# Kernel optimization log

Measured on AMD Instinct MI355X. Metric: run time of the kernel, lower is better.

## Reference

```python
import jax, jax.numpy as jnp
import numpy as np

D = 256       # dim
M = 50        # num_celltypes
NPATH = 65536 # path tokens (256*256)
N = M + NPATH
FF = 3        # focusing_factor
K = 5         # dwc kernel size


def find_closest_factors(num):
    for i in range(int(num ** 0.5), 0, -1):
        if num % i == 0:
            return (i, num // i)
    return (1, num)


def setup_inputs() -> dict:
    key = jax.random.key(0)
    ks = jax.random.split(key, 16)
    def w(k, shape, s=0.02):
        return jax.random.normal(k, shape, dtype=jnp.float32) * s
    z = lambda *s: jnp.zeros(s, jnp.float32)
    return {
        "x": jax.random.normal(ks[0], (1, N, D), dtype=jnp.float32),
        "W_qkv": w(ks[1], (D, 3 * D)),
        "scale_linear": w(ks[2], (1, 1, D)),
        "dwc_w": w(ks[3], (D, 1, K, K)),
        "dwc_b": w(ks[4], (D,)),
        "Wa": w(ks[5], (D, D)), "ba": z(D),
        "Wb": w(ks[6], (D, D)), "bb": z(D),
        "Wc": w(ks[7], (D, 1)), "bc": z(1),
        "W1": w(ks[8], (D, D)), "b1": z(D),
        "W2": w(ks[9], (D, D)), "b2": z(D),
        "W3a": w(ks[10], (2 * D, D)), "b3a": z(D),
        "W3b": w(ks[11], (D, D)), "b3b": z(D),
        "Wf": w(ks[12], (D, D)), "bf": z(D),
    }


def reference(x, W_qkv, scale_linear, dwc_w, dwc_b, Wa, ba, Wb, bb, Wc, bc,
              W1, b1, W2, b2, W3a, b3a, W3b, b3b, Wf, bf):
    scale = D ** -0.5
    qkv = x @ W_qkv                         # (1, N, 3D)
    q, k, v = jnp.split(qkv, 3, axis=-1)
    qc, qp = q[:, :M], q[:, M:]
    kc, kp = k[:, :M], k[:, M:]
    vc, vp = v[:, :M], v[:, M:]

    # --- softmax attention branches ---
    sa = jax.nn.softmax(jnp.einsum('bic,bjc->bij', qc * scale, kc), axis=-1)
    out_self_celltypes = sa @ vc            # (1, M, D)
    cap = jax.nn.softmax(jnp.einsum('bic,bjc->bij', qp * scale, kc), axis=-1)
    out_cross_path = cap @ vc               # (1, NPATH, D)
    cac = jax.nn.softmax(jnp.einsum('bic,bjc->bij', qc * scale, kp), axis=-1)
    out_cross_celltypes = cac @ vp          # (1, M, D)

    # --- focused linear attention on path tokens ---
    sp = jax.nn.softplus(scale_linear)
    ql = (jax.nn.relu(qp) + 1e-6) / sp
    kl = (jax.nn.relu(kp) + 1e-6) / sp
    qn = jnp.linalg.norm(ql, axis=-1, keepdims=True)
    kn = jnp.linalg.norm(kl, axis=-1, keepdims=True)
    ql = ql ** FF
    kl = kl ** FF
    ql = ql / jnp.linalg.norm(ql, axis=-1, keepdims=True) * qn
    kl = kl / jnp.linalg.norm(kl, axis=-1, keepdims=True) * kn
    zfac = 1.0 / (jnp.einsum('bic,bc->bi', ql, kl.sum(axis=1)) + 1e-6)
    kv = jnp.einsum('bjc,bjd->bcd', kl, vp)                 # (1, D, D)
    out_s = jnp.einsum('bic,bcd,bi->bid', ql, kv, zfac)     # (1, NPATH, D)

    # --- depthwise conv feature map ---
    wc, hc = find_closest_factors(NPATH)
    fm = vp.reshape(1, wc, hc, D).transpose(0, 3, 1, 2)     # b c w h
    fm = jax.lax.conv_general_dilated(
        fm, dwc_w, (1, 1), 'SAME',
        dimension_numbers=('NCHW', 'OIHW', 'NCHW'), feature_group_count=D)
    fm = fm + dwc_b[None, :, None, None]
    fm = fm.transpose(0, 2, 3, 1).reshape(1, NPATH, D)
    out_self_path = (out_s + fm) @ Wf + bf  # feamap_linear (dropout=eval)

    # --- gated attention net (shared weights, 4 calls) ---
    def gated(t):
        t = t[0]  # squeeze batch -> (n, D)
        a = jnp.tanh(t @ Wa + ba)
        g = jax.nn.sigmoid(t @ Wb + bb)
        return (a * g) @ Wc + bc  # (n, 1)

    A_cc = gated(out_cross_celltypes)
    A_cp = gated(out_cross_path)
    A_sc = gated(out_self_celltypes)
    A_sp = gated(out_self_path)

    # --- attention fusion (shared weights, 2 calls) ---
    def fuse(A1, A2, x1, x2):
        h1 = jax.nn.softmax(A1.T, axis=1) @ x1[0]   # (1, D)
        h1 = jax.nn.relu(h1 @ W1 + b1)
        h2 = jax.nn.softmax(A2.T, axis=1) @ x2[0]
        h2 = jax.nn.relu(h2 @ W2 + b2)
        f = jnp.concatenate([h1, h2], axis=1)       # (1, 2D)
        return jax.nn.relu(jax.nn.relu(f @ W3a + b3a) @ W3b + b3b)

    fusion_cross = fuse(A_cc, A_cp, out_cross_celltypes, out_cross_path)
    fusion_self = fuse(A_sc, A_sp, out_self_celltypes, out_self_path)
    return jnp.concatenate([fusion_cross, fusion_self], axis=1)  # (1, 2D)
```

## Files before the change

### kernel.cpp

```cpp
#include <hip/hip_runtime.h>
#include <hip/hip_bf16.h>
#include <math.h>


constexpr int DD = 256;
constexpr int MM = 50;
constexpr float SCL = 0.0625f;

constexpr size_t B_VPH = 0;
constexpr size_t B_QLH = (size_t)32 << 20;
constexpr size_t B_KLH = (size_t)64 << 20;
constexpr size_t B_E   = (size_t)96 << 20;
constexpr size_t B_SM  = (size_t)112 << 20;
constexpr size_t B_X   = B_SM + ((size_t)2 << 20);

constexpr size_t KLSUMR = 0;
constexpr size_t KLSUMP = 256;
constexpr size_t OCCDENP= 2304;
constexpr size_t W50P   = 2816;
constexpr size_t EDENP  = 3328;
constexpr size_t H2TP   = 3336;
constexpr size_t H2DENP = 5384;
constexpr size_t OCCRAW = 5392;
constexpr size_t ZEND   = 18192;
constexpr size_t QC     = ZEND;
constexpr size_t KC     = QC + 12800;
constexpr size_t VC     = KC + 12800;
constexpr size_t VCA    = VC + 12800;
constexpr size_t VCB    = VCA + 12800;
constexpr size_t WFA    = VCB + 12800;
constexpr size_t WFB    = WFA + 65536;
constexpr size_t BFA    = WFB + 65536;
constexpr size_t BFB    = BFA + 256;
constexpr size_t OSCB   = BFB + 256;
constexpr size_t OCCB   = OSCB + 12800;
constexpr size_t ASC    = OCCB + 12800;
constexpr size_t ACC50  = ASC + 64;
constexpr size_t SMEND  = ACC50 + 64;

constexpr size_t XT_WQKV = 0;
constexpr size_t XT_WFAT = 196608;
constexpr size_t XT_WFBT = 262144;
constexpr size_t XT_KVT  = 327680;
constexpr size_t XT_QCH  = 393216;
constexpr size_t XT_KCH  = 409600;
constexpr size_t XT_VCAT = 425984;
constexpr size_t XT_VCBT = 442368;
constexpr size_t XT_END  = 458752;
constexpr size_t WS_NEEDED = B_X + XT_END * 2;

typedef short bf16x8 __attribute__((ext_vector_type(8)));
typedef float f32x4 __attribute__((ext_vector_type(4)));

__device__ __forceinline__ float rcpf_(float x){ return __builtin_amdgcn_rcpf(x); }
__device__ __forceinline__ float fsig_(float x){ return rcpf_(1.0f + __expf(-x)); }
__device__ __forceinline__ float ftanh_(float x){ return 1.0f - 2.0f * rcpf_(__expf(2.0f * x) + 1.0f); }

__device__ __forceinline__ float bf2f(unsigned short u){
  return __uint_as_float(((unsigned int)u) << 16);
}
__device__ __forceinline__ unsigned short f2bf(float f){
  union { __hip_bfloat16 h; unsigned short u; } c;
  c.h = __float2bfloat16(f);
  return c.u;
}
__device__ __forceinline__ f32x4 mfma16(bf16x8 a, bf16x8 b, f32x4 c){
  return __builtin_amdgcn_mfma_f32_16x16x32_bf16(a, b, c, 0, 0, 0);
}

__device__ __forceinline__ float waveAllSum(float v){
  #pragma unroll
  for (int m = 1; m < 64; m <<= 1) v += __shfl_xor(v, m, 64);
  return v;
}

__device__ __forceinline__ size_t fragIdx(int n, int k, int K8){
  const int tile = n >> 4, cn = n & 15;
  const int k0 = k >> 5, kqi = (k >> 3) & 3, e = k & 7;
  return (((size_t)tile * K8 + k0) * 64 + (kqi * 16 + cn)) * 8 + e;
}

__device__ __forceinline__ int kvOff(int c, int k){
  return c * 40 + (c >> 3) * 8 + k;
}

__global__ void __launch_bounds__(256) k_prep0(const float* __restrict__ x, const float* __restrict__ Wqkv,
                                               float* qc, float* kc, float* vc,
                                               unsigned short* qch, unsigned short* kch,
                                               unsigned short* __restrict__ WT){
  const int b = blockIdx.x, t = threadIdx.x;
  if (b < 48) {
    __shared__ unsigned short Tt[64][72];
    const int bn = b % 12, bk = b / 12;
    const int n0 = bn * 64, k0g = bk * 64;
    #pragma unroll
    for (int i = 0; i < 16; i++) {
      const int k_l = (t >> 6) + i * 4;
      const int n_l = t & 63;
      Tt[n_l][k_l] = f2bf(Wqkv[(size_t)(k0g + k_l) * 768 + n0 + n_l]);
    }
    __syncthreads();
    #pragma unroll
    for (int i = 0; i < 2; i++) {
      const int fr = t * 2 + i;
      const int t_l = fr >> 7;
      const int k0_l = (fr >> 6) & 1;
      const int lane_f = fr & 63;
      const int n_l = t_l * 16 + (lane_f & 15);
      const int k_l = k0_l * 32 + (lane_f >> 4) * 8;
      const int tg = (n0 >> 4) + t_l;
      const int k0gl = (k0g >> 5) + k0_l;
      bf16x8 v = *(const bf16x8*)&Tt[n_l][k_l];
      *(bf16x8*)&WT[(((size_t)tg * 8 + k0gl) * 64 + lane_f) * 8] = v;
    }
    return;
  }
  __shared__ float xs[256];
  const int r = b - 48, j = t;
  xs[j] = x[r * DD + j];
  __syncthreads();
  float aq = 0.f, ak = 0.f, av = 0.f;
  for (int k = 0; k < DD; k++) {
    float xv = xs[k];
    aq += xv * Wqkv[k * 768 + j];
    ak += xv * Wqkv[k * 768 + 256 + j];
    av += xv * Wqkv[k * 768 + 512 + j];
  }
  qc[r * DD + j] = aq; kc[r * DD + j] = ak; vc[r * DD + j] = av;
  qch[fragIdx(r, j, 8)] = f2bf(aq);
  kch[fragIdx(r, j, 8)] = f2bf(ak);
  if (r == 0) {
    for (int c = 50; c < 64; c++) {
      qch[fragIdx(c, j, 8)] = 0;
      kch[fragIdx(c, j, 8)] = 0;
    }
  }
}

__global__ void __launch_bounds__(256) k_prep1(const float* vc, const float* Wa, const float* Wb,
                                               const float* ba, const float* bb,
                                               const float* Wf, const float* bf,
                                               float* Vca, float* Vcb,
                                               unsigned short* VcaTh, unsigned short* VcbTh,
                                               float* Wfa, float* Wfb, float* bfa, float* bfb,
                                               unsigned short* WfaTh, unsigned short* WfbTh){
  __shared__ float rs[256];
  const int b = blockIdx.x, j = threadIdx.x;
  if (b < 50) {
    const int r = b;
    rs[j] = vc[r * DD + j];
    __syncthreads();
    float a = 0.f, bv = 0.f;
    for (int k = 0; k < DD; k++) { float v = rs[k]; a += v * Wa[k * DD + j]; bv += v * Wb[k * DD + j]; }
    Vca[r * DD + j] = a; Vcb[r * DD + j] = bv;
    VcaTh[fragIdx(j, r, 2)] = f2bf(a);
    VcbTh[fragIdx(j, r, 2)] = f2bf(bv);
    if (r == 0) {
      for (int c = 50; c < 64; c++) {
        VcaTh[fragIdx(j, c, 2)] = 0;
        VcbTh[fragIdx(j, c, 2)] = 0;
      }
    }
    return;
  }
  const int bb2 = b - 50;
  const float* src; const float* Wm;
  if (bb2 < 256)      { src = Wf + bb2 * DD;         Wm = Wa; }
  else if (bb2 < 512) { src = Wf + (bb2 - 256) * DD; Wm = Wb; }
  else if (bb2 == 512){ src = bf;                    Wm = Wa; }
  else                { src = bf;                    Wm = Wb; }
  rs[j] = src[j];
  __syncthreads();
  float a = 0.f;
  for (int k = 0; k < DD; k++) a += rs[k] * Wm[k * DD + j];
  if (bb2 < 256)      { Wfa[bb2 * DD + j] = a; WfaTh[fragIdx(j, bb2, 8)] = f2bf(a); }
  else if (bb2 < 512) { Wfb[(bb2 - 256) * DD + j] = a; WfbTh[fragIdx(j, bb2 - 256, 8)] = f2bf(a); }
  else if (bb2 == 512) bfa[j] = a + ba[j];
  else bfb[j] = a + bb[j];
}

__global__ void __launch_bounds__(256) k_oscg(const float* __restrict__ qc, const float* __restrict__ kc,
                                              const float* __restrict__ vc,
                                              const float* __restrict__ Wa, const float* __restrict__ Wb,
                                              const float* __restrict__ ba, const float* __restrict__ bb,
                                              const float* __restrict__ Wc, const float* __restrict__ bc,
                                              float* __restrict__ osc, float* __restrict__ A){
  const int i = blockIdx.x, t = threadIdx.x;
  __shared__ float qs[256];
  __shared__ float P[64];
  __shared__ float red[4];
  qs[t] = qc[i * DD + t];
  __syncthreads();
  if (t < 64) {
    float s = -1e30f;
    if (t < 50) {
      float acc = 0.f;
      const float4* kr = (const float4*)&kc[t * DD];
      #pragma unroll 8
      for (int k = 0; k < 64; k++) {
        float4 kv = kr[k];
        float4 qv = *(const float4*)&qs[k * 4];
        acc += qv.x * kv.x + qv.y * kv.y + qv.z * kv.z + qv.w * kv.w;
      }
      s = acc * SCL;
    }
    float mx = s;
    #pragma unroll
    for (int m = 1; m < 64; m <<= 1) mx = fmaxf(mx, __shfl_xor(mx, m, 64));
    float e = (t < 50) ? __expf(s - mx) : 0.f;
    float den = waveAllSum(e);
    P[t] = e * rcpf_(den);
  }
  __syncthreads();
  float a = 0.f;
  for (int jj = 0; jj < 50; jj++) a += P[jj] * vc[jj * DD + t];
  osc[i * DD + t] = a;
  __syncthreads();
  qs[t] = a;
  __syncthreads();
  float u = 0.f, v = 0.f;
  for (int k = 0; k < DD; k++) { float tv = qs[k]; u += tv * Wa[k * DD + t]; v += tv * Wb[k * DD + t]; }
  float g = ftanh_(u + ba[t]) * fsig_(v + bb[t]) * Wc[t];
  g = waveAllSum(g);
  const int lane = t & 63, wv = t >> 6;
  if (lane == 0) red[wv] = g;
  __syncthreads();
  if (t == 0) A[i] = red[0] + red[1] + red[2] + red[3] + bc[0];
}

__global__ void __launch_bounds__(256) k_gated(const float* __restrict__ tin,
                                               const float* __restrict__ Wa, const float* __restrict__ Wb,
                                               const float* __restrict__ ba, const float* __restrict__ bb,
                                               const float* __restrict__ Wc, const float* __restrict__ bc,
                                               float* __restrict__ A){
  int r = blockIdx.x, j = threadIdx.x;
  __shared__ float ts[256];
  __shared__ float red[4];
  ts[j] = tin[r * DD + j];
  __syncthreads();
  float u = 0.f, v = 0.f;
  for (int k = 0; k < DD; k++) { float tv = ts[k]; u += tv * Wa[k * DD + j]; v += tv * Wb[k * DD + j]; }
  float g = ftanh_(u + ba[j]) * fsig_(v + bb[j]) * Wc[j];
  g = waveAllSum(g);
  int lane = j & 63, wv = j >> 6;
  if (lane == 0) red[wv] = g;
  __syncthreads();
  if (j == 0) A[r] = red[0] + red[1] + red[2] + red[3] + bc[0];
}

__global__ void __launch_bounds__(256) k_path1(
    const float* __restrict__ x, const unsigned short* __restrict__ WTf,
    const float* __restrict__ sln,
    const unsigned short* __restrict__ kchf, const unsigned short* __restrict__ qchf,
    const unsigned short* __restrict__ VcaTf, const unsigned short* __restrict__ VcbTf,
    const float* __restrict__ ba, const float* __restrict__ bb,
    const float* __restrict__ Wc, const float* __restrict__ bc,
    unsigned short* __restrict__ vph, unsigned short* __restrict__ qlh, unsigned short* __restrict__ klh,
    float* __restrict__ E, float* __restrict__ w50p, float* __restrict__ edenp, float* __restrict__ occdenp){
  __shared__ __align__(16) char arena[38912];
  unsigned short (*Psh)[72]   = (unsigned short (*)[72])arena;
  float (*denp)[4]            = (float (*)[4])(arena + 4608);
  unsigned short (*qpsb)[264] = (unsigned short (*)[264])(arena + 5120);
  unsigned short (*kpsb)[264] = (unsigned short (*)[264])(arena + 22016);

  const int tid = threadIdx.x;
  const int i0 = blockIdx.x * 32;
  const int part = blockIdx.x & 7;
  const int lane = tid & 63;
  const int wvv = tid >> 6;
  const int cn = lane & 15;
  const int m0 = (lane >> 4) * 4;
  const int kq = (lane >> 4) * 8;

  for (int l = tid; l < 2048; l += 256) {
    const int r = l >> 6, c4 = (l & 63) * 4;
    const float4 xv = *(const float4*)&x[(size_t)(MM + i0 + r) * DD + c4];
    ushort4 o; o.x = f2bf(xv.x); o.y = f2bf(xv.y); o.z = f2bf(xv.z); o.w = f2bf(xv.w);
    *(ushort4*)&qpsb[r][c4] = o;
  }
  __syncthreads();

  bf16x8 af0[8], af1[8];
  #pragma unroll
  for (int k0 = 0; k0 < 8; k0++) {
    af0[k0] = *(const bf16x8*)&qpsb[cn][k0 * 32 + kq];
    af1[k0] = *(const bf16x8*)&qpsb[16 + cn][k0 * 32 + kq];
  }
  __syncthreads();

  bf16x8 b0[8], b1[8];
  {
    const unsigned short* Bt = WTf + ((size_t)wvv * 8 * 64 + lane) * 8;
    #pragma unroll
    for (int k0 = 0; k0 < 8; k0++) b0[k0] = *(const bf16x8*)&Bt[(size_t)k0 * 512];
  }
  #pragma unroll 1
  for (int tt = 0; tt < 12; tt++) {
    const int t = wvv + 4 * tt;
    if (tt + 1 < 12) {
      const unsigned short* Bt = WTf + (((size_t)(t + 4) * 8) * 64 + lane) * 8;
      #pragma unroll
      for (int k0 = 0; k0 < 8; k0++) b1[k0] = *(const bf16x8*)&Bt[(size_t)k0 * 512];
    }
    f32x4 acc0 = {0.f, 0.f, 0.f, 0.f};
    f32x4 acc1 = {0.f, 0.f, 0.f, 0.f};
    #pragma unroll
    for (int k0 = 0; k0 < 8; k0++) {
      acc0 = mfma16(af0[k0], b0[k0], acc0);
      acc1 = mfma16(af1[k0], b0[k0], acc1);
    }
    if (t < 16) {
      int c = t * 16 + cn;
      #pragma unroll
      for (int i = 0; i < 4; i++) {
        qpsb[m0 + i][c] = f2bf(acc0[i]);
        qpsb[16 + m0 + i][c] = f2bf(acc1[i]);
      }
    } else if (t < 32) {
      int c = (t - 16) * 16 + cn;
      #pragma unroll
      for (int i = 0; i < 4; i++) {
        kpsb[m0 + i][c] = f2bf(acc0[i]);
        kpsb[16 + m0 + i][c] = f2bf(acc1[i]);
      }
    } else {
      int c = (t - 32) * 16 + cn;
      #pragma unroll
      for (int i = 0; i < 4; i++) {
        vph[(size_t)(i0 + m0 + i) * DD + c] = f2bf(acc0[i]);
        vph[(size_t)(i0 + 16 + m0 + i) * DD + c] = f2bf(acc1[i]);
      }
    }
    #pragma unroll
    for (int k0 = 0; k0 < 8; k0++) b0[k0] = b1[k0];
  }
  __syncthreads();

  float ep0[4], ep1[4];
  {
    f32x4 accp0 = {0.f,0.f,0.f,0.f}, accp1 = {0.f,0.f,0.f,0.f};
    f32x4 accc0 = {0.f,0.f,0.f,0.f}, accc1 = {0.f,0.f,0.f,0.f};
    const unsigned short* Bk = kchf + ((size_t)wvv * 8 * 64 + lane) * 8;
    const unsigned short* Bq = qchf + ((size_t)wvv * 8 * 64 + lane) * 8;
    #pragma unroll
    for (int k0 = 0; k0 < 8; k0++) {
      bf16x8 aq0 = *(const bf16x8*)&qpsb[cn][k0 * 32 + kq];
      bf16x8 aq1 = *(const bf16x8*)&qpsb[16 + cn][k0 * 32 + kq];
      bf16x8 ak0 = *(const bf16x8*)&kpsb[cn][k0 * 32 + kq];
      bf16x8 ak1 = *(const bf16x8*)&kpsb[16 + cn][k0 * 32 + kq];
      bf16x8 bk = *(const bf16x8*)&Bk[(size_t)k0 * 512];
      bf16x8 bq = *(const bf16x8*)&Bq[(size_t)k0 * 512];
      accp0 = mfma16(aq0, bk, accp0);
      accp1 = mfma16(aq1, bk, accp1);
      accc0 = mfma16(ak0, bq, accc0);
      accc1 = mfma16(ak1, bq, accc1);
    }
    const int col = wvv * 16 + cn;
    const bool ok = (col < 50);
    #pragma unroll
    for (int i = 0; i < 4; i++) {
      ep0[i] = ok ? __expf(accp0[i] * SCL) : 0.f;
      ep1[i] = ok ? __expf(accp1[i] * SCL) : 0.f;
    }
    float osum = 0.f;
    #pragma unroll
    for (int i = 0; i < 4; i++) {
      float ec0 = __expf(accc0[i] * SCL);
      float ec1 = __expf(accc1[i] * SCL);
      E[(size_t)(i0 + m0 + i) * 64 + col] = ok ? ec0 : 0.f;
      E[(size_t)(i0 + 16 + m0 + i) * 64 + col] = ok ? ec1 : 0.f;
      if (ok) osum += ec0 + ec1;
    }
    osum += __shfl_xor(osum, 16, 64);
    osum += __shfl_xor(osum, 32, 64);
    if (lane < 16 && ok) atomicAdd(&occdenp[part * 64 + col], osum);
    float d0[4], d1[4];
    #pragma unroll
    for (int i = 0; i < 4; i++) { d0[i] = ep0[i]; d1[i] = ep1[i]; }
    #pragma unroll
    for (int m = 1; m < 16; m <<= 1) {
      #pragma unroll
      for (int i = 0; i < 4; i++) {
        d0[i] += __shfl_xor(d0[i], m, 64);
        d1[i] += __shfl_xor(d1[i], m, 64);
      }
    }
    if (cn == 0) {
      #pragma unroll
      for (int i = 0; i < 4; i++) {
        denp[m0 + i][wvv] = d0[i];
        denp[16 + m0 + i][wvv] = d1[i];
      }
    }
  }
  __syncthreads();

  {
    const int col = wvv * 16 + cn;
    #pragma unroll
    for (int i = 0; i < 4; i++) {
      float4 dp = *(const float4*)&denp[m0 + i][0];
      Psh[m0 + i][col] = f2bf(ep0[i] * rcpf_(dp.x + dp.y + dp.z + dp.w));
      float4 dq = *(const float4*)&denp[16 + m0 + i][0];
      Psh[16 + m0 + i][col] = f2bf(ep1[i] * rcpf_(dq.x + dq.y + dq.z + dq.w));
    }
  }

  float4 sl4 = ((const float4*)sln)[lane];
  float4 rsp;
  rsp.x = rcpf_(log1pf(expf(sl4.x))); rsp.y = rcpf_(log1pf(expf(sl4.y)));
  rsp.z = rcpf_(log1pf(expf(sl4.z))); rsp.w = rcpf_(log1pf(expf(sl4.w)));
  float4 ba4 = ((const float4*)ba)[lane];
  float4 bb4 = ((const float4*)bb)[lane];
  float4 wc4 = ((const float4*)Wc)[lane];
  float bcv = bc[0];
  for (int rr = 0; rr < 8; rr++) {
    const int r = wvv * 8 + rr;
    const int row = i0 + r;
    ushort4 qu = *(const ushort4*)&qpsb[r][lane * 4];
    ushort4 ku = *(const ushort4*)&kpsb[r][lane * 4];
    float4 q4 = {bf2f(qu.x), bf2f(qu.y), bf2f(qu.z), bf2f(qu.w)};
    float4 k4 = {bf2f(ku.x), bf2f(ku.y), bf2f(ku.z), bf2f(ku.w)};
    float4 lq, lk;
    lq.x = (fmaxf(q4.x, 0.f) + 1e-6f) * rsp.x; lq.y = (fmaxf(q4.y, 0.f) + 1e-6f) * rsp.y;
    lq.z = (fmaxf(q4.z, 0.f) + 1e-6f) * rsp.z; lq.w = (fmaxf(q4.w, 0.f) + 1e-6f) * rsp.w;
    lk.x = (fmaxf(k4.x, 0.f) + 1e-6f) * rsp.x; lk.y = (fmaxf(k4.y, 0.f) + 1e-6f) * rsp.y;
    lk.z = (fmaxf(k4.z, 0.f) + 1e-6f) * rsp.z; lk.w = (fmaxf(k4.w, 0.f) + 1e-6f) * rsp.w;
    float4 q3, k3;
    q3.x = lq.x*lq.x*lq.x; q3.y = lq.y*lq.y*lq.y; q3.z = lq.z*lq.z*lq.z; q3.w = lq.w*lq.w*lq.w;
    k3.x = lk.x*lk.x*lk.x; k3.y = lk.y*lk.y*lk.y; k3.z = lk.z*lk.z*lk.z; k3.w = lk.w*lk.w*lk.w;
    float n1q = lq.x*lq.x + lq.y*lq.y + lq.z*lq.z + lq.w*lq.w;
    float n3q = q3.x*q3.x + q3.y*q3.y + q3.z*q3.z + q3.w*q3.w;
    float n1k = lk.x*lk.x + lk.y*lk.y + lk.z*lk.z + lk.w*lk.w;
    float n3k = k3.x*k3.x + k3.y*k3.y + k3.z*k3.z + k3.w*k3.w;
    n1q = waveAllSum(n1q); n3q = waveAllSum(n3q);
    n1k = waveAllSum(n1k); n3k = waveAllSum(n3k);
    float fq = sqrtf(n1q * rcpf_(n3q));
    float fk = sqrtf(n1k * rcpf_(n3k));
    ushort4 qo, ko;
    qo.x = f2bf(q3.x * fq); qo.y = f2bf(q3.y * fq); qo.z = f2bf(q3.z * fq); qo.w = f2bf(q3.w * fq);
    ko.x = f2bf(k3.x * fk); ko.y = f2bf(k3.y * fk); ko.z = f2bf(k3.z * fk); ko.w = f2bf(k3.w * fk);
    *(ushort4*)&qlh[(size_t)row * DD + lane * 4] = qo;
    *(ushort4*)&klh[(size_t)row * DD + lane * 4] = ko;
  }
  __syncthreads();

  {
    bf16x8 ap0[2], ap1[2];
    #pragma unroll
    for (int k0 = 0; k0 < 2; k0++) {
      ap0[k0] = *(const bf16x8*)&Psh[cn][k0 * 32 + kq];
      ap1[k0] = *(const bf16x8*)&Psh[16 + cn][k0 * 32 + kq];
    }
    #pragma unroll 1
    for (int tt = 0; tt < 4; tt++) {
      const int nt = wvv * 4 + tt;
      const unsigned short* Bu = VcaTf + (((size_t)nt * 2) * 64 + lane) * 8;
      const unsigned short* Bv = VcbTf + (((size_t)nt * 2) * 64 + lane) * 8;
      f32x4 au0 = {0.f,0.f,0.f,0.f}, au1 = {0.f,0.f,0.f,0.f};
      f32x4 av0 = {0.f,0.f,0.f,0.f}, av1 = {0.f,0.f,0.f,0.f};
      #pragma unroll
      for (int k0 = 0; k0 < 2; k0++) {
        bf16x8 bu = *(const bf16x8*)&Bu[(size_t)k0 * 512];
        bf16x8 bv = *(const bf16x8*)&Bv[(size_t)k0 * 512];
        au0 = mfma16(ap0[k0], bu, au0);
        au1 = mfma16(ap1[k0], bu, au1);
        av0 = mfma16(ap0[k0], bv, av0);
        av1 = mfma16(ap1[k0], bv, av1);
      }
      #pragma unroll
      for (int i = 0; i < 4; i++) {
        qpsb[m0 + i][nt * 16 + cn] = f2bf(au0[i]);
        qpsb[16 + m0 + i][nt * 16 + cn] = f2bf(au1[i]);
        kpsb[m0 + i][nt * 16 + cn] = f2bf(av0[i]);
        kpsb[16 + m0 + i][nt * 16 + cn] = f2bf(av1[i]);
      }
    }
  }
  __syncthreads();

  #pragma unroll
  for (int rr = 0; rr < 8; rr++) {
    const int r = wvv * 8 + rr;
    ushort4 uu = *(const ushort4*)&qpsb[r][lane * 4];
    ushort4 vv = *(const ushort4*)&kpsb[r][lane * 4];
    float g = ftanh_(bf2f(uu.x) + ba4.x) * fsig_(bf2f(vv.x) + bb4.x) * wc4.x
            + ftanh_(bf2f(uu.y) + ba4.y) * fsig_(bf2f(vv.y) + bb4.y) * wc4.y
            + ftanh_(bf2f(uu.z) + ba4.z) * fsig_(bf2f(vv.z) + bb4.z) * wc4.z
            + ftanh_(bf2f(uu.w) + ba4.w) * fsig_(bf2f(vv.w) + bb4.w) * wc4.w;
    g = waveAllSum(g);
    if (lane == 0) *(float*)&Psh[r][64] = __expf(g + bcv);
  }
  __syncthreads();
  if (tid < 64) {
    float s = 0.f;
    #pragma unroll
    for (int r = 0; r < 32; r++) s += *(const float*)&Psh[r][64] * bf2f(Psh[r][tid]);
    atomicAdd(&w50p[part * 64 + tid], s);
  }
  if (tid == 0) {
    float es = 0.f;
    #pragma unroll
    for (int r = 0; r < 32; r++) es += *(const float*)&Psh[r][64];
    atomicAdd(&edenp[part], es);
  }
}

__global__ void __launch_bounds__(512) k_occnum(const float* __restrict__ E, const unsigned short* __restrict__ vph,
                                                float* __restrict__ occraw){
  const int d = threadIdx.x & 255;
  const int half = threadIdx.x >> 8;
  const int j0 = blockIdx.x * 256;
  __shared__ float Es[2][32][64];
  float acc[52];
  #pragma unroll
  for (int i = 0; i < 52; i++) acc[i] = 0.f;
  for (int s = 0; s < 4; s++) {
    const int sj = j0 + (half * 4 + s) * 32;
    for (int l = d; l < 512; l += 256) {
      int jj = l >> 4, cq = l & 15;
      *(float4*)&Es[half][jj][cq * 4] = ((const float4*)(E + (size_t)(sj + jj) * 64))[cq];
    }
    __syncthreads();
    for (int jj = 0; jj < 32; jj++) {
      float vv = bf2f(vph[(size_t)(sj + jj) * DD + d]);
      #pragma unroll
      for (int q = 0; q < 13; q++) {
        float4 e4 = *(const float4*)&Es[half][jj][q * 4];
        acc[q * 4 + 0] += e4.x * vv; acc[q * 4 + 1] += e4.y * vv;
        acc[q * 4 + 2] += e4.z * vv; acc[q * 4 + 3] += e4.w * vv;
      }
    }
    __syncthreads();
  }
  for (int i = 0; i < 50; i++) atomicAdd(&occraw[i * DD + d], acc[i]);
}

__global__ void __launch_bounds__(256) k_kv(const unsigned short* __restrict__ klh,
                                            const unsigned short* __restrict__ vph,
                                            unsigned short* __restrict__ PP,
                                            float* __restrict__ klsump){
  __shared__ __align__(16) unsigned short AklT[2608];
  __shared__ __align__(16) unsigned short BvpT[10480];
  const int tid = threadIdx.x;
  const int lane = tid & 63;
  const int wvv = tid >> 6;
  const int cn = lane & 15;
  const int m0 = (lane >> 4) * 4;
  const int kq = (lane >> 4) * 8;
  const int cb = blockIdx.x;
  const int z  = blockIdx.y;
  const int jj = tid >> 3;
  const int c8 = (tid & 7) * 8;

  f32x4 acc[4][4];
  f32x4 acc1[4];
  #pragma unroll
  for (int mt = 0; mt < 4; mt++) {
    acc1[mt] = (f32x4){0.f,0.f,0.f,0.f};
    #pragma unroll
    for (int tl = 0; tl < 4; tl++) acc[mt][tl] = (f32x4){0.f,0.f,0.f,0.f};
  }
  bf16x8 ones;
  #pragma unroll
  for (int i = 0; i < 8; i++) ones[i] = (short)0x3F80;

  const int jbase = z * 512;
  #pragma unroll 1
  for (int step = 0; step < 16; step++) {
    const int j0 = jbase + step * 32;
    {
      bf16x8 av = *(const bf16x8*)&klh[(size_t)(j0 + jj) * 256 + cb * 64 + c8];
      #pragma unroll
      for (int i = 0; i < 8; i++) AklT[kvOff(c8 + i, jj)] = (unsigned short)av[i];
      #pragma unroll
      for (int rep = 0; rep < 4; rep++) {
        bf16x8 bv = *(const bf16x8*)&vph[(size_t)(j0 + jj) * 256 + rep * 64 + c8];
        #pragma unroll
        for (int i = 0; i < 8; i++) BvpT[kvOff(rep * 64 + c8 + i, jj)] = (unsigned short)bv[i];
      }
    }
    __syncthreads();
    bf16x8 afr[4], bfr[4];
    #pragma unroll
    for (int mt = 0; mt < 4; mt++)
      afr[mt] = *(const bf16x8*)&AklT[kvOff(cn + mt * 16, kq)];
    #pragma unroll
    for (int tl = 0; tl < 4; tl++)
      bfr[tl] = *(const bf16x8*)&BvpT[kvOff(wvv * 64 + tl * 16 + cn, kq)];
    #pragma unroll
    for (int mt = 0; mt < 4; mt++) {
      acc1[mt] = mfma16(afr[mt], ones, acc1[mt]);
      #pragma unroll
      for (int tl = 0; tl < 4; tl++) acc[mt][tl] = mfma16(afr[mt], bfr[tl], acc[mt][tl]);
    }
    __syncthreads();
  }
  unsigned short* P = PP + ((size_t)(cb * 128 + z)) * 16384;
  #pragma unroll
  for (int mt = 0; mt < 4; mt++)
    #pragma unroll
    for (int tl = 0; tl < 4; tl++) {
      const int n = (wvv * 4 + tl) * 16 + cn;
      #pragma unroll
      for (int i = 0; i < 4; i++)
        P[(size_t)(mt * 16 + m0 + i) * 256 + n] = f2bf(acc[mt][tl][i]);
    }
  if (wvv == 0 && cn == 0) {
    #pragma unroll
    for (int mt = 0; mt < 4; mt++)
      #pragma unroll
      for (int i = 0; i < 4; i++)
        atomicAdd(&klsump[(z & 7) * 256 + cb * 64 + mt * 16 + m0 + i], acc1[mt][i]);
  }
}

__global__ void __launch_bounds__(256) k_fin2(const unsigned short* __restrict__ PP,
                                              unsigned short* __restrict__ kvTf,
                                              const float* __restrict__ occraw,
                                              const float* __restrict__ occdenp,
                                              float* __restrict__ occ,
                                              const float* __restrict__ klsump,
                                              float* __restrict__ klsum){
  const int b = blockIdx.x, d = threadIdx.x;
  if (b < 256) {
    const int cb = b >> 6, m = b & 63;
    float s = 0.f;
    for (int z = 0; z < 128; z++)
      s += bf2f(PP[((size_t)(cb * 128 + z)) * 16384 + (size_t)m * 256 + d]);
    kvTf[fragIdx(d, b, 8)] = f2bf(s);
  } else if (b < 306) {
    const int i = b - 256;
    float den = 0.f;
    #pragma unroll
    for (int p = 0; p < 8; p++) den += occdenp[p * 64 + i];
    occ[i * DD + d] = occraw[i * DD + d] / den;
  } else {
    float s = 0.f;
    #pragma unroll
    for (int p = 0; p < 8; p++) s += klsump[p * 256 + d];
    klsum[d] = s;
  }
}

__global__ void __launch_bounds__(256) k_tail(const unsigned short* __restrict__ qlh,
                                              const unsigned short* __restrict__ kvTf,
                                              const float* __restrict__ klsum,
                                              const unsigned short* __restrict__ vph,
                                              const float* __restrict__ dwcw, const float* __restrict__ dwcb,
                                              const unsigned short* __restrict__ WfaTf,
                                              const unsigned short* __restrict__ WfbTf,
                                              const float* __restrict__ bfa, const float* __restrict__ bfb,
                                              const float* __restrict__ Wc, const float* __restrict__ bc,
                                              float* __restrict__ h2tp, float* __restrict__ h2denp){
  __shared__ unsigned short Tsh[32][264];
  __shared__ unsigned short OSb[32][264];
  __shared__ unsigned short aVb[32][264];
  __shared__ float zf[32];
  __shared__ float ev[32];
  const int tid = threadIdx.x;
  const int i0 = blockIdx.x * 32;
  const int part = blockIdx.x & 7;
  const int lane = tid & 63;
  const int wvv = tid >> 6;
  const int cn = lane & 15;
  const int m0 = (lane >> 4) * 4;
  const int kq = (lane >> 4) * 8;
  for (int l = tid; l < 2048; l += 256) {
    int r = l >> 6, c4 = (l & 63) * 4;
    *(ushort4*)&Tsh[r][c4] = *(const ushort4*)&qlh[(size_t)(i0 + r) * DD + c4];
  }
  __syncthreads();
  {
    bf16x8 afq0[8], afq1[8];
    #pragma unroll
    for (int k0 = 0; k0 < 8; k0++) {
      afq0[k0] = *(const bf16x8*)&Tsh[cn][k0 * 32 + kq];
      afq1[k0] = *(const bf16x8*)&Tsh[16 + cn][k0 * 32 + kq];
    }
    #pragma unroll 1
    for (int tt = 0; tt < 4; tt++) {
      const int nt = wvv * 4 + tt;
      const unsigned short* Bt = kvTf + (((size_t)nt * 8) * 64 + lane) * 8;
      f32x4 acc0 = {0.f,0.f,0.f,0.f};
      f32x4 acc1 = {0.f,0.f,0.f,0.f};
      #pragma unroll
      for (int k0 = 0; k0 < 8; k0++) {
        bf16x8 b = *(const bf16x8*)&Bt[(size_t)k0 * 512];
        acc0 = mfma16(afq0[k0], b, acc0);
        acc1 = mfma16(afq1[k0], b, acc1);
      }
      #pragma unroll
      for (int i = 0; i < 4; i++) {
        OSb[m0 + i][nt * 16 + cn] = f2bf(acc0[i]);
        OSb[16 + m0 + i][nt * 16 + cn] = f2bf(acc1[i]);
      }
    }
  }
  {
    float4 ks4 = ((const float4*)klsum)[lane];
    #pragma unroll
    for (int rr = 0; rr < 8; rr++) {
      const int r = wvv * 8 + rr;
      ushort4 q4 = *(const ushort4*)&Tsh[r][lane * 4];
      float s = bf2f(q4.x)*ks4.x + bf2f(q4.y)*ks4.y + bf2f(q4.z)*ks4.z + bf2f(q4.w)*ks4.w;
      s = waveAllSum(s);
      if (lane == 0) zf[r] = rcpf_(s + 1e-6f);
    }
  }
  __syncthreads();
  const int j = tid;
  float w[25];
  #pragma unroll
  for (int t = 0; t < 25; t++) w[t] = dwcw[j * 25 + t];
  const float bias = dwcb[j];
  const int y = i0 >> 8, x0 = i0 & 255;
  float fm[32];
  #pragma unroll
  for (int r = 0; r < 32; r++) fm[r] = bias;
  #pragma unroll
  for (int dy = -2; dy <= 2; dy++) {
    const int yy = y + dy;
    if ((unsigned)yy > 255u) continue;
    float buf[36];
    #pragma unroll
    for (int i = 0; i < 36; i++) {
      const int xx = x0 - 2 + i;
      buf[i] = ((unsigned)xx <= 255u) ? bf2f(vph[(size_t)((yy << 8) + xx) * DD + j]) : 0.f;
    }
    const float* wr = &w[(dy + 2) * 5];
    #pragma unroll
    for (int r = 0; r < 32; r++)
      fm[r] += buf[r] * wr[0] + buf[r+1] * wr[1] + buf[r+2] * wr[2]
             + buf[r+3] * wr[3] + buf[r+4] * wr[4];
  }
  #pragma unroll
  for (int r = 0; r < 32; r++) {
    fm[r] = bf2f(OSb[r][j]) * zf[r] + fm[r];
    Tsh[r][j] = f2bf(fm[r]);
  }
  __syncthreads();
  {
    bf16x8 aft0[8], aft1[8];
    #pragma unroll
    for (int k0 = 0; k0 < 8; k0++) {
      aft0[k0] = *(const bf16x8*)&Tsh[cn][k0 * 32 + kq];
      aft1[k0] = *(const bf16x8*)&Tsh[16 + cn][k0 * 32 + kq];
    }
    #pragma unroll 1
    for (int jb = 0; jb < 8; jb++) {
      const int nt = wvv * 4 + (jb & 3);
      const unsigned short* Bt = ((jb < 4) ? WfaTf : WfbTf) + (((size_t)nt * 8) * 64 + lane) * 8;
      f32x4 acc0 = {0.f,0.f,0.f,0.f};
      f32x4 acc1 = {0.f,0.f,0.f,0.f};
      #pragma unroll
      for (int k0 = 0; k0 < 8; k0++) {
        bf16x8 b = *(const bf16x8*)&Bt[(size_t)k0 * 512];
        acc0 = mfma16(aft0[k0], b, acc0);
        acc1 = mfma16(aft1[k0], b, acc1);
      }
      unsigned short (*dst)[264] = (jb < 4) ? OSb : aVb;
      #pragma unroll
      for (int i = 0; i < 4; i++) {
        dst[m0 + i][nt * 16 + cn] = f2bf(acc0[i]);
        dst[16 + m0 + i][nt * 16 + cn] = f2bf(acc1[i]);
      }
    }
  }
  __syncthreads();
  {
    float4 bfa4 = ((const float4*)bfa)[lane];
    float4 bfb4 = ((const float4*)bfb)[lane];
    float4 wc4 = ((const float4*)Wc)[lane];
    const float bcv = bc[0];
    #pragma unroll
    for (int rr = 0; rr < 8; rr++) {
      const int r = wvv * 8 + rr;
      ushort4 uu = *(const ushort4*)&OSb[r][lane * 4];
      ushort4 vv = *(const ushort4*)&aVb[r][lane * 4];
      float g = ftanh_(bf2f(uu.x) + bfa4.x) * fsig_(bf2f(vv.x) + bfb4.x) * wc4.x
              + ftanh_(bf2f(uu.y) + bfa4.y) * fsig_(bf2f(vv.y) + bfb4.y) * wc4.y
              + ftanh_(bf2f(uu.z) + bfa4.z) * fsig_(bf2f(vv.z) + bfb4.z) * wc4.z
              + ftanh_(bf2f(uu.w) + bfa4.w) * fsig_(bf2f(vv.w) + bfb4.w) * wc4.w;
      g = waveAllSum(g);
      if (lane == 0) ev[r] = __expf(g + bcv);
    }
  }
  __syncthreads();
  float hp = 0.f;
  #pragma unroll
  for (int r = 0; r < 32; r++) hp += ev[r] * fm[r];
  atomicAdd(&h2tp[part * 256 + j], hp);
  if (tid == 0) {
    float es = 0.f;
    #pragma unroll
    for (int r = 0; r < 32; r++) es += ev[r];
    atomicAdd(&h2denp[part], es);
  }
}

__global__ void __launch_bounds__(256) k_final(
    const float* __restrict__ A_cc, const float* __restrict__ occ,
    const float* __restrict__ A_sc, const float* __restrict__ osc,
    const float* __restrict__ w50p, const float* __restrict__ edenp,
    const float* __restrict__ h2tp, const float* __restrict__ h2denp,
    const float* __restrict__ vc, const float* __restrict__ Wf, const float* __restrict__ bf,
    const float* __restrict__ W1, const float* __restrict__ b1,
    const float* __restrict__ W2, const float* __restrict__ b2,
    const float* __restrict__ W3a, const float* __restrict__ b3a,
    const float* __restrict__ W3b, const float* __restrict__ b3b,
    float* __restrict__ out){
  int j = threadIdx.x;
  __shared__ float pw[64];
  __shared__ float w50t[64];
  __shared__ float t1[256], t2[256], h1[256], h2[256], fz[512], z1[256];
  if (j < 64) {
    float s = 0.f;
    #pragma unroll
    for (int p = 0; p < 8; p++) s += w50p[p * 64 + j];
    w50t[j] = s;
  }
  float edentot = 0.f, h2dentot = 0.f;
  #pragma unroll
  for (int p = 0; p < 8; p++) { edentot += edenp[p]; h2dentot += h2denp[p]; }
  if (j < 64) pw[j] = (j < 50) ? expf(A_cc[j]) : 0.f;
  __syncthreads();
  float den = 0.f;
  for (int i = 0; i < 50; i++) den += pw[i];
  float raw = 0.f;
  for (int i = 0; i < 50; i++) raw += pw[i] * occ[i * DD + j];
  t1[j] = raw / den;
  float r2 = 0.f;
  for (int i = 0; i < 50; i++) r2 += w50t[i] * vc[i * DD + j];
  t2[j] = r2 / edentot;
  __syncthreads();
  float a1 = 0.f, a2 = 0.f;
  for (int k = 0; k < DD; k++) { a1 += t1[k] * W1[k * DD + j]; a2 += t2[k] * W2[k * DD + j]; }
  h1[j] = fmaxf(a1 + b1[j], 0.f);
  h2[j] = fmaxf(a2 + b2[j], 0.f);
  __syncthreads();
  fz[j] = h1[j]; fz[256 + j] = h2[j];
  __syncthreads();
  float z = 0.f;
  for (int k = 0; k < 512; k++) z += fz[k] * W3a[k * DD + j];
  z1[j] = fmaxf(z + b3a[j], 0.f);
  __syncthreads();
  float o = 0.f;
  for (int k = 0; k < DD; k++) o += z1[k] * W3b[k * DD + j];
  out[j] = fmaxf(o + b3b[j], 0.f);
  __syncthreads();
  if (j < 64) pw[j] = (j < 50) ? expf(A_sc[j]) : 0.f;
  __syncthreads();
  den = 0.f;
  for (int i = 0; i < 50; i++) den += pw[i];
  raw = 0.f;
  for (int i = 0; i < 50; i++) raw += pw[i] * osc[i * DD + j];
  t1[j] = raw / den;
  {
    float s = 0.f;
    #pragma unroll
    for (int p = 0; p < 8; p++) s += h2tp[p * 256 + j];
    t2[j] = s / h2dentot;
  }
  __syncthreads();
  float hs = 0.f;
  for (int k = 0; k < DD; k++) hs += t2[k] * Wf[k * DD + j];
  __syncthreads();
  t2[j] = hs + bf[j];
  __syncthreads();
  a1 = 0.f; a2 = 0.f;
  for (int k = 0; k < DD; k++) { a1 += t1[k] * W1[k * DD + j]; a2 += t2[k] * W2[k * DD + j]; }
  h1[j] = fmaxf(a1 + b1[j], 0.f);
  h2[j] = fmaxf(a2 + b2[j], 0.f);
  __syncthreads();
  fz[j] = h1[j]; fz[256 + j] = h2[j];
  __syncthreads();
  z = 0.f;
  for (int k = 0; k < 512; k++) z += fz[k] * W3a[k * DD + j];
  z1[j] = fmaxf(z + b3a[j], 0.f);
  __syncthreads();
  o = 0.f;
  for (int k = 0; k < DD; k++) o += z1[k] * W3b[k * DD + j];
  out[256 + j] = fmaxf(o + b3b[j], 0.f);
}

extern "C" void kernel_launch(void* const* d_in, const int* in_sizes, int n_in,
                              void* d_out, int out_size, void* d_ws, size_t ws_size,
                              hipStream_t stream) {
  if (ws_size < WS_NEEDED) return;
  const float* x   = (const float*)d_in[0];
  const float* Wqkv= (const float*)d_in[1];
  const float* sln = (const float*)d_in[2];
  const float* dwcw= (const float*)d_in[3];
  const float* dwcb= (const float*)d_in[4];
  const float* Wa  = (const float*)d_in[5];
  const float* ba  = (const float*)d_in[6];
  const float* Wb  = (const float*)d_in[7];
  const float* bb  = (const float*)d_in[8];
  const float* Wc  = (const float*)d_in[9];
  const float* bc  = (const float*)d_in[10];
  const float* W1  = (const float*)d_in[11];
  const float* b1  = (const float*)d_in[12];
  const float* W2  = (const float*)d_in[13];
  const float* b2  = (const float*)d_in[14];
  const float* W3a = (const float*)d_in[15];
  const float* b3a = (const float*)d_in[16];
  const float* W3b = (const float*)d_in[17];
  const float* b3b = (const float*)d_in[18];
  const float* Wf  = (const float*)d_in[19];
  const float* bf  = (const float*)d_in[20];

  char* wsb = (char*)d_ws;
  unsigned short* VPH = (unsigned short*)(wsb + B_VPH);
  unsigned short* QLH = (unsigned short*)(wsb + B_QLH);
  unsigned short* KLH = (unsigned short*)(wsb + B_KLH);
  float* EB = (float*)(wsb + B_E);
  float* SM = (float*)(wsb + B_SM);
  unsigned short* XT = (unsigned short*)(wsb + B_X);
  float* outp = (float*)d_out;

  hipMemsetAsync((void*)SM, 0, ZEND * sizeof(float), stream);

  k_prep0<<<98, 256, 0, stream>>>(x, Wqkv, SM + QC, SM + KC, SM + VC,
                                  XT + XT_QCH, XT + XT_KCH, XT + XT_WQKV);
  k_prep1<<<564, 256, 0, stream>>>(SM + VC, Wa, Wb, ba, bb, Wf, bf,
                                   SM + VCA, SM + VCB, XT + XT_VCAT, XT + XT_VCBT,
                                   SM + WFA, SM + WFB, SM + BFA, SM + BFB,
                                   XT + XT_WFAT, XT + XT_WFBT);
  k_oscg<<<50, 256, 0, stream>>>(SM + QC, SM + KC, SM + VC, Wa, Wb, ba, bb, Wc, bc,
                                 SM + OSCB, SM + ASC);

  k_path1<<<2048, 256, 0, stream>>>(x, XT + XT_WQKV, sln, XT + XT_KCH, XT + XT_QCH,
                                    XT + XT_VCAT, XT + XT_VCBT, ba, bb, Wc, bc,
                                    VPH, QLH, KLH, EB, SM + W50P, SM + EDENP, SM + OCCDENP);
  k_occnum<<<256, 512, 0, stream>>>(EB, VPH, SM + OCCRAW);
  k_kv<<<dim3(4, 128), 256, 0, stream>>>(KLH, VPH, (unsigned short*)EB, SM + KLSUMP);
  k_fin2<<<307, 256, 0, stream>>>((const unsigned short*)EB, XT + XT_KVT,
                                  SM + OCCRAW, SM + OCCDENP, SM + OCCB,
                                  SM + KLSUMP, SM + KLSUMR);
  k_gated<<<50, 256, 0, stream>>>(SM + OCCB, Wa, Wb, ba, bb, Wc, bc, SM + ACC50);

  k_tail<<<2048, 256, 0, stream>>>(QLH, XT + XT_KVT, SM + KLSUMR, VPH, dwcw, dwcb,
                                   XT + XT_WFAT, XT + XT_WFBT, SM + BFA, SM + BFB,
                                   Wc, bc, SM + H2TP, SM + H2DENP);

  k_final<<<1, 256, 0, stream>>>(SM + ACC50, SM + OCCB, SM + ASC, SM + OSCB,
                                 SM + W50P, SM + EDENP, SM + H2TP, SM + H2DENP,
                                 SM + VC, Wf, bf, W1, b1, W2, b2, W3a, b3a, W3b, b3b, outp);
}
```

Before: 574.7 us.

## Store softmax exponentials in bf16 and compute occnum with MFMA tiles

k_path1 now writes the cross-attention exponentials E as bf16 instead of fp32, halving that buffer's write and read traffic. The row sums are taken from the rounded values so numerator and denominator stay consistent. k_occnum drops its scalar FMA loop over fp32 E and instead stages E and vp into transposed LDS tiles and accumulates with bf16 MFMA, then atomically adds the partial results. The Wf·Wa/Wb precompute also moves from k_prep1 into k_prep0, so k_prep1 only handles the vc-dependent rows. The cost is bf16 rounding of the exponentials, which loses some precision.

```diff
diff --git a/kernel.cpp b/kernel.cpp
--- a/kernel.cpp
+++ b/kernel.cpp
@@ -87,7 +87,12 @@
 __global__ void __launch_bounds__(256) k_prep0(const float* __restrict__ x, const float* __restrict__ Wqkv,
                                                float* qc, float* kc, float* vc,
                                                unsigned short* qch, unsigned short* kch,
-                                               unsigned short* __restrict__ WT){
+                                               unsigned short* __restrict__ WT,
+                                               const float* __restrict__ Wa, const float* __restrict__ Wb,
+                                               const float* __restrict__ ba, const float* __restrict__ bb,
+                                               const float* __restrict__ Wf, const float* __restrict__ bf,
+                                               float* Wfa, float* Wfb, float* bfa, float* bfb,
+                                               unsigned short* WfaTh, unsigned short* WfbTh){
   const int b = blockIdx.x, t = threadIdx.x;
   if (b < 48) {
     __shared__ unsigned short Tt[64][72];
@@ -116,67 +121,64 @@
     return;
   }
   __shared__ float xs[256];
-  const int r = b - 48, j = t;
-  xs[j] = x[r * DD + j];
-  __syncthreads();
-  float aq = 0.f, ak = 0.f, av = 0.f;
-  for (int k = 0; k < DD; k++) {
-    float xv = xs[k];
-    aq += xv * Wqkv[k * 768 + j];
-    ak += xv * Wqkv[k * 768 + 256 + j];
-    av += xv * Wqkv[k * 768 + 512 + j];
-  }
-  qc[r * DD + j] = aq; kc[r * DD + j] = ak; vc[r * DD + j] = av;
-  qch[fragIdx(r, j, 8)] = f2bf(aq);
-  kch[fragIdx(r, j, 8)] = f2bf(ak);
-  if (r == 0) {
-    for (int c = 50; c < 64; c++) {
-      qch[fragIdx(c, j, 8)] = 0;
-      kch[fragIdx(c, j, 8)] = 0;
-    }
-  }
-}
-
-__global__ void __launch_bounds__(256) k_prep1(const float* vc, const float* Wa, const float* Wb,
-                                               const float* ba, const float* bb,
-                                               const float* Wf, const float* bf,
-                                               float* Vca, float* Vcb,
-                                               unsigned short* VcaTh, unsigned short* VcbTh,
-                                               float* Wfa, float* Wfb, float* bfa, float* bfb,
-                                               unsigned short* WfaTh, unsigned short* WfbTh){
-  __shared__ float rs[256];
-  const int b = blockIdx.x, j = threadIdx.x;
-  if (b < 50) {
-    const int r = b;
-    rs[j] = vc[r * DD + j];
+  const int j = t;
+  if (b < 98) {
+    const int r = b - 48;
+    xs[j] = x[r * DD + j];
     __syncthreads();
-    float a = 0.f, bv = 0.f;
-    for (int k = 0; k < DD; k++) { float v = rs[k]; a += v * Wa[k * DD + j]; bv += v * Wb[k * DD + j]; }
-    Vca[r * DD + j] = a; Vcb[r * DD + j] = bv;
-    VcaTh[fragIdx(j, r, 2)] = f2bf(a);
-    VcbTh[fragIdx(j, r, 2)] = f2bf(bv);
+    float aq = 0.f, ak = 0.f, av = 0.f;
+    for (int k = 0; k < DD; k++) {
+      float xv = xs[k];
+      aq += xv * Wqkv[k * 768 + j];
+      ak += xv * Wqkv[k * 768 + 256 + j];
+      av += xv * Wqkv[k * 768 + 512 + j];
+    }
+    qc[r * DD + j] = aq; kc[r * DD + j] = ak; vc[r * DD + j] = av;
+    qch[fragIdx(r, j, 8)] = f2bf(aq);
+    kch[fragIdx(r, j, 8)] = f2bf(ak);
     if (r == 0) {
       for (int c = 50; c < 64; c++) {
-        VcaTh[fragIdx(j, c, 2)] = 0;
-        VcbTh[fragIdx(j, c, 2)] = 0;
+        qch[fragIdx(c, j, 8)] = 0;
+        kch[fragIdx(c, j, 8)] = 0;
       }
     }
     return;
   }
-  const int bb2 = b - 50;
+  const int bb2 = b - 98;
   const float* src; const float* Wm;
   if (bb2 < 256)      { src = Wf + bb2 * DD;         Wm = Wa; }
   else if (bb2 < 512) { src = Wf + (bb2 - 256) * DD; Wm = Wb; }
   else if (bb2 == 512){ src = bf;                    Wm = Wa; }
   else                { src = bf;                    Wm = Wb; }
-  rs[j] = src[j];
+  xs[j] = src[j];
   __syncthreads();
   float a = 0.f;
-  for (int k = 0; k < DD; k++) a += rs[k] * Wm[k * DD + j];
+  for (int k = 0; k < DD; k++) a += xs[k] * Wm[k * DD + j];
   if (bb2 < 256)      { Wfa[bb2 * DD + j] = a; WfaTh[fragIdx(j, bb2, 8)] = f2bf(a); }
   else if (bb2 < 512) { Wfb[(bb2 - 256) * DD + j] = a; WfbTh[fragIdx(j, bb2 - 256, 8)] = f2bf(a); }
   else if (bb2 == 512) bfa[j] = a + ba[j];
   else bfb[j] = a + bb[j];
+}
+
+__global__ void __launch_bounds__(256) k_prep1(const float* vc, const float* Wa, const float* Wb,
+                                               float* Vca, float* Vcb,
+                                               unsigned short* VcaTh, unsigned short* VcbTh){
+  __shared__ float rs[256];
+  const int b = blockIdx.x, j = threadIdx.x;
+  const int r = b;
+  rs[j] = vc[r * DD + j];
+  __syncthreads();
+  float a = 0.f, bv = 0.f;
+  for (int k = 0; k < DD; k++) { float v = rs[k]; a += v * Wa[k * DD + j]; bv += v * Wb[k * DD + j]; }
+  Vca[r * DD + j] = a; Vcb[r * DD + j] = bv;
+  VcaTh[fragIdx(j, r, 2)] = f2bf(a);
+  VcbTh[fragIdx(j, r, 2)] = f2bf(bv);
+  if (r == 0) {
+    for (int c = 50; c < 64; c++) {
+      VcaTh[fragIdx(j, c, 2)] = 0;
+      VcbTh[fragIdx(j, c, 2)] = 0;
+    }
+  }
 }
 
 __global__ void __launch_bounds__(256) k_oscg(const float* __restrict__ qc, const float* __restrict__ kc,
@@ -256,7 +258,7 @@
     const float* __restrict__ ba, const float* __restrict__ bb,
     const float* __restrict__ Wc, const float* __restrict__ bc,
     unsigned short* __restrict__ vph, unsigned short* __restrict__ qlh, unsigned short* __restrict__ klh,
-    float* __restrict__ E, float* __restrict__ w50p, float* __restrict__ edenp, float* __restrict__ occdenp){
+    unsigned short* __restrict__ Eh, float* __restrict__ w50p, float* __restrict__ edenp, float* __restrict__ occdenp){
   __shared__ __align__(16) char arena[38912];
   unsigned short (*Psh)[72]   = (unsigned short (*)[72])arena;
   float (*denp)[4]            = (float (*)[4])(arena + 4608);
@@ -365,11 +367,11 @@
     float osum = 0.f;
     #pragma unroll
     for (int i = 0; i < 4; i++) {
-      float ec0 = __expf(accc0[i] * SCL);
-      float ec1 = __expf(accc1[i] * SCL);
-      E[(size_t)(i0 + m0 + i) * 64 + col] = ok ? ec0 : 0.f;
-      E[(size_t)(i0 + 16 + m0 + i) * 64 + col] = ok ? ec1 : 0.f;
-      if (ok) osum += ec0 + ec1;
+      unsigned short h0 = ok ? f2bf(__expf(accc0[i] * SCL)) : (unsigned short)0;
+      unsigned short h1 = ok ? f2bf(__expf(accc1[i] * SCL)) : (unsigned short)0;
+      Eh[(size_t)(i0 + m0 + i) * 64 + col] = h0;
+      Eh[(size_t)(i0 + 16 + m0 + i) * 64 + col] = h1;
+      if (ok) osum += bf2f(h0) + bf2f(h1);
     }
     osum += __shfl_xor(osum, 16, 64);
     osum += __shfl_xor(osum, 32, 64);
@@ -506,34 +508,69 @@
   }
 }
 
-__global__ void __launch_bounds__(512) k_occnum(const float* __restrict__ E, const unsigned short* __restrict__ vph,
+__global__ void __launch_bounds__(256) k_occnum(const unsigned short* __restrict__ Eh,
+                                                const unsigned short* __restrict__ vph,
                                                 float* __restrict__ occraw){
-  const int d = threadIdx.x & 255;
-  const int half = threadIdx.x >> 8;
-  const int j0 = blockIdx.x * 256;
-  __shared__ float Es[2][32][64];
-  float acc[52];
-  #pragma unroll
-  for (int i = 0; i < 52; i++) acc[i] = 0.f;
-  for (int s = 0; s < 4; s++) {
-    const int sj = j0 + (half * 4 + s) * 32;
-    for (int l = d; l < 512; l += 256) {
-      int jj = l >> 4, cq = l & 15;
-      *(float4*)&Es[half][jj][cq * 4] = ((const float4*)(E + (size_t)(sj + jj) * 64))[cq];
+  __shared__ __align__(16) unsigned short EhT[2608];
+  __shared__ __align__(16) unsigned short BvpT[10480];
+  const int tid = threadIdx.x;
+  const int lane = tid & 63;
+  const int wvv = tid >> 6;
+  const int cn = lane & 15;
+  const int m0 = (lane >> 4) * 4;
+  const int kq = (lane >> 4) * 8;
+  const int z  = blockIdx.x;
+  const int jj = tid >> 3;
+  const int c8 = (tid & 7) * 8;
+
+  f32x4 acc[4][4];
+  #pragma unroll
+  for (int mt = 0; mt < 4; mt++)
+    #pragma unroll
+    for (int tl = 0; tl < 4; tl++) acc[mt][tl] = (f32x4){0.f,0.f,0.f,0.f};
+
+  const int jbase = z * 512;
+  #pragma unroll 1
+  for (int step = 0; step < 16; step++) {
+    const int j0 = jbase + step * 32;
+    {
+      bf16x8 av = *(const bf16x8*)&Eh[(size_t)(j0 + jj) * 64 + c8];
+      #pragma unroll
+      for (int i = 0; i < 8; i++) EhT[kvOff(c8 + i, jj)] = (unsigned short)av[i];
+      #pragma unroll
+      for (int rep = 0; rep < 4; rep++) {
+        bf16x8 bv = *(const bf16x8*)&vph[(size_t)(j0 + jj) * 256 + rep * 64 + c8];
+        #pragma unroll
+        for (int i = 0; i < 8; i++) BvpT[kvOff(rep * 64 + c8 + i, jj)] = (unsigned short)bv[i];
+      }
     }
     __syncthreads();
-    for (int jj = 0; jj < 32; jj++) {
-      float vv = bf2f(vph[(size_t)(sj + jj) * DD + d]);
-      #pragma unroll
-      for (int q = 0; q < 13; q++) {
-        float4 e4 = *(const float4*)&Es[half][jj][q * 4];
-        acc[q * 4 + 0] += e4.x * vv; acc[q * 4 + 1] += e4.y * vv;
-        acc[q * 4 + 2] += e4.z * vv; acc[q * 4 + 3] += e4.w * vv;
-      }
-    }
+    bf16x8 afr[4], bfr[4];
+    #pragma unroll
+    for (int mt = 0; mt < 4; mt++)
+      afr[mt] = *(const bf16x8*)&EhT[kvOff(cn + mt * 16, kq)];
+    #pragma unroll
+    for (int tl = 0; tl < 4; tl++)
+      bfr[tl] = *(const bf16x8*)&BvpT[kvOff(wvv * 64 + tl * 16 + cn, kq)];
+    #pragma unroll
+    for (int mt = 0; mt < 4; mt++)
+      #pragma unroll
+      for (int tl = 0; tl < 4; tl++) acc[mt][tl] = mfma16(afr[mt], bfr[tl], acc[mt][tl]);
     __syncthreads();
   }
-  for (int i = 0; i < 50; i++) atomicAdd(&occraw[i * DD + d], acc[i]);
+  #pragma unroll
+  for (int mt = 0; mt < 4; mt++)
+    #pragma unroll
+    for (int i = 0; i < 4; i++) {
+      const int ri = mt * 16 + m0 + i;
+      if (ri < 50) {
+        #pragma unroll
+        for (int tl = 0; tl < 4; tl++) {
+          const int d = wvv * 64 + tl * 16 + cn;
+          atomicAdd(&occraw[ri * DD + d], acc[mt][tl][i]);
+        }
+      }
+    }
 }
 
 __global__ void __launch_bounds__(256) k_kv(const unsigned short* __restrict__ klh,
@@ -914,28 +951,29 @@
   unsigned short* VPH = (unsigned short*)(wsb + B_VPH);
   unsigned short* QLH = (unsigned short*)(wsb + B_QLH);
   unsigned short* KLH = (unsigned short*)(wsb + B_KLH);
-  float* EB = (float*)(wsb + B_E);
+  unsigned short* EHB = (unsigned short*)(wsb + B_E);
   float* SM = (float*)(wsb + B_SM);
   unsigned short* XT = (unsigned short*)(wsb + B_X);
   float* outp = (float*)d_out;
 
   hipMemsetAsync((void*)SM, 0, ZEND * sizeof(float), stream);
 
-  k_prep0<<<98, 256, 0, stream>>>(x, Wqkv, SM + QC, SM + KC, SM + VC,
-                                  XT + XT_QCH, XT + XT_KCH, XT + XT_WQKV);
-  k_prep1<<<564, 256, 0, stream>>>(SM + VC, Wa, Wb, ba, bb, Wf, bf,
-                                   SM + VCA, SM + VCB, XT + XT_VCAT, XT + XT_VCBT,
+  k_prep0<<<612, 256, 0, stream>>>(x, Wqkv, SM + QC, SM + KC, SM + VC,
+                                   XT + XT_QCH, XT + XT_KCH, XT + XT_WQKV,
+                                   Wa, Wb, ba, bb, Wf, bf,
                                    SM + WFA, SM + WFB, SM + BFA, SM + BFB,
                                    XT + XT_WFAT, XT + XT_WFBT);
+  k_prep1<<<50, 256, 0, stream>>>(SM + VC, Wa, Wb,
+                                  SM + VCA, SM + VCB, XT + XT_VCAT, XT + XT_VCBT);
   k_oscg<<<50, 256, 0, stream>>>(SM + QC, SM + KC, SM + VC, Wa, Wb, ba, bb, Wc, bc,
                                  SM + OSCB, SM + ASC);
 
   k_path1<<<2048, 256, 0, stream>>>(x, XT + XT_WQKV, sln, XT + XT_KCH, XT + XT_QCH,
                                     XT + XT_VCAT, XT + XT_VCBT, ba, bb, Wc, bc,
-                                    VPH, QLH, KLH, EB, SM + W50P, SM + EDENP, SM + OCCDENP);
-  k_occnum<<<256, 512, 0, stream>>>(EB, VPH, SM + OCCRAW);
-  k_kv<<<dim3(4, 128), 256, 0, stream>>>(KLH, VPH, (unsigned short*)EB, SM + KLSUMP);
-  k_fin2<<<307, 256, 0, stream>>>((const unsigned short*)EB, XT + XT_KVT,
+                                    VPH, QLH, KLH, EHB, SM + W50P, SM + EDENP, SM + OCCDENP);
+  k_occnum<<<128, 256, 0, stream>>>(EHB, VPH, SM + OCCRAW);
+  k_kv<<<dim3(4, 128), 256, 0, stream>>>(KLH, VPH, EHB, SM + KLSUMP);
+  k_fin2<<<307, 256, 0, stream>>>(EHB, XT + XT_KVT,
                                   SM + OCCRAW, SM + OCCDENP, SM + OCCB,
                                   SM + KLSUMP, SM + KLSUMR);
   k_gated<<<50, 256, 0, stream>>>(SM + OCCB, Wa, Wb, ba, bb, Wc, bc, SM + ACC50);
```

New measurement: 528.4 us. -8.1%, faster.
